# Performance work log

Hardware: AMD Instinct MI355X
Metric: run time of the kernel (lower is better)

## Reference

```python
import jax, jax.numpy as jnp
import numpy as np
import math

B, S, D = 1, 4096, 512
H, KVH, DH = 8, 4, 64
DH2 = DH // 2
M = int(math.isqrt(S))           # product-key grid side, S == M*M
K = 8                            # top_k
ROPE_BASE = 10000.0


def rope_cos_sin(seq_len, dh, base):
    inv_freq = 1.0 / (base ** (jnp.arange(0, dh, 2, dtype=jnp.float32) / dh))
    t = jnp.arange(seq_len, dtype=jnp.float32)
    freqs = jnp.outer(t, inv_freq)                      # (S, dh/2)
    emb = jnp.concatenate([freqs, freqs], axis=-1)      # (S, dh)
    return jnp.cos(emb), jnp.sin(emb)


def apply_rope(x, cos, sin):
    # x: (B, H, S, dh); half-split rotation (llama-style)
    dh2 = x.shape[-1] // 2
    rot = jnp.concatenate([-x[..., dh2:], x[..., :dh2]], axis=-1)
    return x * cos + rot * sin


def setup_inputs() -> dict:
    key = jax.random.key(0)
    ks = jax.random.split(key, 5)
    s = 0.02
    x = jax.random.normal(ks[0], (B, S, D), dtype=jnp.float32)
    Wq = jax.random.normal(ks[1], (H * DH, D), dtype=jnp.float32) * s
    Wk = jax.random.normal(ks[2], (KVH * DH, D), dtype=jnp.float32) * s
    Wv = jax.random.normal(ks[3], (KVH * DH, D), dtype=jnp.float32) * s
    Wo = jax.random.normal(ks[4], (D, H * DH), dtype=jnp.float32) * s
    return {"x": x, "Wq": Wq, "Wk": Wk, "Wv": Wv, "Wo": Wo}


def reference(x, Wq, Wk, Wv, Wo):
    b, s, d = x.shape
    cos, sin = rope_cos_sin(s, DH, ROPE_BASE)
    q = (x @ Wq.T).reshape(b, s, H, DH).transpose(0, 2, 1, 3)      # (B,H,S,DH)
    k = (x @ Wk.T).reshape(b, s, KVH, DH).transpose(0, 2, 1, 3)    # (B,KVH,S,DH)
    v = (x @ Wv.T).reshape(b, s, KVH, DH).transpose(0, 2, 1, 3)
    q = apply_rope(q, cos, sin)
    k = apply_rope(k, cos, sin)
    rep = H // KVH                                                 # GQA repeat_kv
    k = jnp.repeat(k, rep, axis=1)                                 # (B,H,S,DH)
    v = jnp.repeat(v, rep, axis=1)

    # factorized product keys: sum over grid rows / cols
    kg = k.reshape(b, H, M, M, DH)
    k1 = kg[..., :DH2].sum(axis=-2)                                # (B,H,M,DH2)
    k2 = kg[..., DH2:].sum(axis=-3)                                # (B,H,M,DH2)
    q1, q2 = q[..., :DH2], q[..., DH2:]

    def topk_sel(qh, kh):  # qh: (S,DH2), kh: (M,DH2)
        scores = qh @ kh.T                                         # (S,M)
        _, idx = jax.lax.top_k(scores, K)                          # (S,K)
        return kh[idx], idx                                        # (S,K,DH2), (S,K)

    sel2 = jax.vmap(jax.vmap(topk_sel))
    k1v, i1 = sel2(q1, k1)                                         # (B,H,S,K,DH2)
    k2v, i2 = sel2(q2, k2)

    # cross-product candidates: (B,H,S,K,K,DH) -> (B,H,S,K*K,DH)
    c1 = jnp.broadcast_to(k1v[:, :, :, :, None, :], (b, H, s, K, K, DH2))
    c2 = jnp.broadcast_to(k2v[:, :, :, None, :, :], (b, H, s, K, K, DH2))
    cand = jnp.concatenate([c1, c2], axis=-1).reshape(b, H, s, K * K, DH)

    scores_final = jnp.einsum('bhsd,bhscd->bhsc', q, cand)         # (B,H,S,K*K)
    _, sel = jax.lax.top_k(scores_final, K)                        # (B,H,S,K)
    final_k = jnp.take_along_axis(cand, sel[..., None], axis=3)    # (B,H,S,K,DH)

    row = jnp.take_along_axis(i1, sel // K, axis=3)
    col = jnp.take_along_axis(i2, sel % K, axis=3)
    v_idx = row * M + col                                          # (B,H,S,K)
    final_v = jax.vmap(jax.vmap(lambda vb, ib: vb[ib]))(v, v_idx)  # (B,H,S,K,DH)

    attn = jax.nn.softmax(
        jnp.einsum('bhsd,bhskd->bhsk', q, final_k) / math.sqrt(DH), axis=-1)
    o = jnp.einsum('bhsk,bhskd->bhsd', attn, final_v)              # (B,H,S,DH)
    o = o.transpose(0, 2, 1, 3).reshape(b, s, H * DH)
    return o @ Wo.T
```

## Files before the change

### kernel.cpp

```cpp
#include <hip/hip_runtime.h>
#include <math.h>


static constexpr size_t OFF_P1   = 0;
static constexpr size_t OFF_P2   = 4194304;
static constexpr size_t OFF_KB   = 8388608;
static constexpr size_t OFF_V    = 9437184;
static constexpr size_t OFF_COS  = 10485760;
static constexpr size_t OFF_SIN  = 10616832;
static constexpr size_t OFF_K1   = 10747904;
static constexpr size_t OFF_K2   = 10756096;
static constexpr size_t OFF_O    = 10764288;
static constexpr size_t OFF_PACK = 12861440;

#define LDB 132
#define TILE_F (16 * LDB)

__device__ __forceinline__ float rdlane_f(float v, int lane) {
  return __int_as_float(__builtin_amdgcn_readlane(__float_as_int(v), lane));
}

__global__ __launch_bounds__(512) void pre_kernel(const float* __restrict__ A,
    const float* __restrict__ Wq, const float* __restrict__ Wk,
    const float* __restrict__ Wv, float* __restrict__ C1,
    float* __restrict__ C2, float* __restrict__ cosT,
    float* __restrict__ sinT) {
  __shared__ float As[2 * TILE_F];
  __shared__ float Bs[2 * TILE_F];
  const int bid = blockIdx.x;
  const int tid = threadIdx.x;
  if (bid >= 512) {
    int idx = (bid - 512) * 512 + tid;
    int s = idx >> 5;
    int dp = idx & 31;
    double e = (double)dp * (1.0 / 32.0);
    float pf = (float)pow(10000.0, e);
    float invf = 1.0f / pf;
    float argf = __fmul_rn((float)s, invf);
    cosT[idx] = (float)cos((double)argf);
    sinT[idx] = (float)sin((double)argf);
    return;
  }
  const int bn = bid & 7;
  const int bm = (bid >> 3) & 31;
  const int z = bid >> 8;
  const int k0 = z ? 384 : 0;
  const int k1 = z ? 512 : 384;
  float* __restrict__ C = z ? C2 : C1;
  const int lrow = tid >> 2;
  const int lko = (tid & 3) << 2;
  const int ty = tid >> 4;
  const int tx = tid & 15;
  const float* Bbase = (bn < 4) ? (Wq + ((size_t)bn * 128) * 512)
                     : (bn < 6) ? (Wk + ((size_t)(bn - 4) * 128) * 512)
                                : (Wv + ((size_t)(bn - 6) * 128) * 512);
  const float* Ap = A + (size_t)(bm * 128 + lrow) * 512 + lko;
  const float* Bp = Bbase + (size_t)lrow * 512 + lko;
  float acc[4][8] = {{0.f}};
  float4 a0 = *(const float4*)(Ap + k0);
  float4 b0 = *(const float4*)(Bp + k0);
  int p = 0;
  for (int kt = k0; kt < k1; kt += 16) {
    float* Asp = As + p * TILE_F;
    float* Bsp = Bs + p * TILE_F;
    Asp[(lko + 0) * LDB + lrow] = a0.x;
    Asp[(lko + 1) * LDB + lrow] = a0.y;
    Asp[(lko + 2) * LDB + lrow] = a0.z;
    Asp[(lko + 3) * LDB + lrow] = a0.w;
    Bsp[(lko + 0) * LDB + lrow] = b0.x;
    Bsp[(lko + 1) * LDB + lrow] = b0.y;
    Bsp[(lko + 2) * LDB + lrow] = b0.z;
    Bsp[(lko + 3) * LDB + lrow] = b0.w;
    __syncthreads();
    if (kt + 16 < k1) {
      a0 = *(const float4*)(Ap + kt + 16);
      b0 = *(const float4*)(Bp + kt + 16);
    }
    #pragma unroll
    for (int k = 0; k < 16; ++k) {
      float4 av = *(const float4*)(&Asp[k * LDB + (ty << 2)]);
      float4 bl = *(const float4*)(&Bsp[k * LDB + (tx << 2)]);
      float4 bh = *(const float4*)(&Bsp[k * LDB + 64 + (tx << 2)]);
      float af[4] = {av.x, av.y, av.z, av.w};
      float bf[8] = {bl.x, bl.y, bl.z, bl.w, bh.x, bh.y, bh.z, bh.w};
      #pragma unroll
      for (int i2 = 0; i2 < 4; ++i2)
        #pragma unroll
        for (int j2 = 0; j2 < 8; ++j2)
          acc[i2][j2] = fmaf(af[i2], bf[j2], acc[i2][j2]);
    }
    p ^= 1;
  }
  #pragma unroll
  for (int i2 = 0; i2 < 4; ++i2) {
    int row = bm * 128 + (ty << 2) + i2;
    float* Cp = C + (size_t)row * 1024 + bn * 128;
    *(float4*)(Cp + (tx << 2))      = make_float4(acc[i2][0], acc[i2][1], acc[i2][2], acc[i2][3]);
    *(float4*)(Cp + 64 + (tx << 2)) = make_float4(acc[i2][4], acc[i2][5], acc[i2][6], acc[i2][7]);
  }
}

__global__ __launch_bounds__(256) void gemm128_out(const float* __restrict__ A,
    const float* __restrict__ B, float* __restrict__ Cbase, int N) {
  __shared__ float As[2 * TILE_F];
  __shared__ float Bs[2 * TILE_F];
  const int tid = threadIdx.x;
  const int z = blockIdx.z;
  const int k0 = z << 7;
  const int k1 = k0 + 128;
  float* __restrict__ C = Cbase + (size_t)z * ((size_t)4096 * N);
  const int bm = blockIdx.y, bn = blockIdx.x;
  const int lrow = tid >> 1;
  const int lko = (tid & 1) << 3;
  const int ty = tid >> 4;
  const int tx = tid & 15;
  const float* Ap = A + (size_t)(bm * 128 + lrow) * 512 + lko;
  const float* Bp = B + (size_t)(bn * 128 + lrow) * 512 + lko;
  float acc[8][8] = {{0.f}};
  float4 a0 = *(const float4*)(Ap + k0);
  float4 a1 = *(const float4*)(Ap + k0 + 4);
  float4 b0 = *(const float4*)(Bp + k0);
  float4 b1 = *(const float4*)(Bp + k0 + 4);
  int p = 0;
  for (int kt = k0; kt < k1; kt += 16) {
    float* Asp = As + p * TILE_F;
    float* Bsp = Bs + p * TILE_F;
    Asp[(lko + 0) * LDB + lrow] = a0.x;
    Asp[(lko + 1) * LDB + lrow] = a0.y;
    Asp[(lko + 2) * LDB + lrow] = a0.z;
    Asp[(lko + 3) * LDB + lrow] = a0.w;
    Asp[(lko + 4) * LDB + lrow] = a1.x;
    Asp[(lko + 5) * LDB + lrow] = a1.y;
    Asp[(lko + 6) * LDB + lrow] = a1.z;
    Asp[(lko + 7) * LDB + lrow] = a1.w;
    Bsp[(lko + 0) * LDB + lrow] = b0.x;
    Bsp[(lko + 1) * LDB + lrow] = b0.y;
    Bsp[(lko + 2) * LDB + lrow] = b0.z;
    Bsp[(lko + 3) * LDB + lrow] = b0.w;
    Bsp[(lko + 4) * LDB + lrow] = b1.x;
    Bsp[(lko + 5) * LDB + lrow] = b1.y;
    Bsp[(lko + 6) * LDB + lrow] = b1.z;
    Bsp[(lko + 7) * LDB + lrow] = b1.w;
    __syncthreads();
    if (kt + 16 < k1) {
      a0 = *(const float4*)(Ap + kt + 16);
      a1 = *(const float4*)(Ap + kt + 20);
      b0 = *(const float4*)(Bp + kt + 16);
      b1 = *(const float4*)(Bp + kt + 20);
    }
    #pragma unroll
    for (int k = 0; k < 16; ++k) {
      float4 al = *(const float4*)(&Asp[k * LDB + (ty << 2)]);
      float4 ah = *(const float4*)(&Asp[k * LDB + 64 + (ty << 2)]);
      float4 bl = *(const float4*)(&Bsp[k * LDB + (tx << 2)]);
      float4 bh = *(const float4*)(&Bsp[k * LDB + 64 + (tx << 2)]);
      float af[8] = {al.x, al.y, al.z, al.w, ah.x, ah.y, ah.z, ah.w};
      float bf[8] = {bl.x, bl.y, bl.z, bl.w, bh.x, bh.y, bh.z, bh.w};
      #pragma unroll
      for (int i2 = 0; i2 < 8; ++i2)
        #pragma unroll
        for (int j2 = 0; j2 < 8; ++j2)
          acc[i2][j2] = fmaf(af[i2], bf[j2], acc[i2][j2]);
    }
    p ^= 1;
  }
  #pragma unroll
  for (int i2 = 0; i2 < 8; ++i2) {
    int row = bm * 128 + ((i2 < 4) ? (ty << 2) + i2 : 64 + (ty << 2) + i2 - 4);
    float* Cp = C + (size_t)row * N + bn * 128;
    *(float4*)(Cp + (tx << 2))      = make_float4(acc[i2][0], acc[i2][1], acc[i2][2], acc[i2][3]);
    *(float4*)(Cp + 64 + (tx << 2)) = make_float4(acc[i2][4], acc[i2][5], acc[i2][6], acc[i2][7]);
  }
}

__global__ __launch_bounds__(256) void combine4_kernel(const float* __restrict__ o0,
    const float* __restrict__ o1, const float* __restrict__ o2,
    const float* __restrict__ o3, float* __restrict__ out) {
  int i = blockIdx.x * 256 + threadIdx.x;
  float4 a = ((const float4*)o0)[i];
  float4 b = ((const float4*)o1)[i];
  float4 c = ((const float4*)o2)[i];
  float4 d = ((const float4*)o3)[i];
  float4 r;
  r.x = __fadd_rn(__fadd_rn(__fadd_rn(a.x, b.x), c.x), d.x);
  r.y = __fadd_rn(__fadd_rn(__fadd_rn(a.y, b.y), c.y), d.y);
  r.z = __fadd_rn(__fadd_rn(__fadd_rn(a.z, b.z), c.z), d.z);
  r.w = __fadd_rn(__fadd_rn(__fadd_rn(a.w, b.w), c.w), d.w);
  ((float4*)out)[i] = r;
}

__global__ __launch_bounds__(64) void k12_rope_kernel(const float* __restrict__ p1,
    const float* __restrict__ p2, const float* __restrict__ cosT,
    const float* __restrict__ sinT, float* __restrict__ k1t,
    float* __restrict__ k2t) {
  int id = blockIdx.x * 64 + threadIdx.x;
  int which = id >> 13;
  int rem = id & 8191;
  int kvh = rem >> 11;
  int rem2 = rem & 2047;
  int i = rem2 >> 5;
  int d = rem2 & 31;
  if (which == 0) {
    float acc = 0.f;
    for (int c = 0; c < 64; ++c) {
      int s = i * 64 + c;
      int idx = (s << 10) + 512 + (kvh << 6) + d;
      float val = __fadd_rn(p1[idx], p2[idx]);
      float pv  = __fadd_rn(p1[idx + 32], p2[idx + 32]);
      float cs = cosT[(s << 5) + d];
      float sn = sinT[(s << 5) + d];
      float out = __fadd_rn(__fmul_rn(val, cs), __fmul_rn(-pv, sn));
      acc = (c == 0) ? out : __fadd_rn(acc, out);
    }
    k1t[(kvh * 64 + i) * 32 + d] = acc;
  } else {
    float acc = 0.f;
    for (int r = 0; r < 64; ++r) {
      int s = r * 64 + i;
      int idx = (s << 10) + 512 + (kvh << 6) + d + 32;
      float val = __fadd_rn(p1[idx], p2[idx]);
      float pv  = __fadd_rn(p1[idx - 32], p2[idx - 32]);
      float cs = cosT[(s << 5) + d];
      float sn = sinT[(s << 5) + d];
      float out = __fadd_rn(__fmul_rn(val, cs), __fmul_rn(pv, sn));
      acc = (r == 0) ? out : __fadd_rn(acc, out);
    }
    k2t[(kvh * 64 + i) * 32 + d] = acc;
  }
}

__global__ __launch_bounds__(256) void stage1_sel_kernel(
    const float* __restrict__ p1, const float* __restrict__ p2,
    const float* __restrict__ cosT, const float* __restrict__ sinT,
    const float* __restrict__ k1t, const float* __restrict__ k2t,
    unsigned long long* __restrict__ packs, float* __restrict__ vb) {
  __shared__ float smem[8704];
  const int bid = blockIdx.x;
  const int t = threadIdx.x;
  if (bid >= 512) {
    int vid = (bid - 512) * 256 + t;
    int s = vid >> 6;
    int g = vid & 63;
    int n = 768 + (g << 2);
    int idx = (s << 10) + n;
    const float4 v1 = *(const float4*)(p1 + idx);
    const float4 v2 = *(const float4*)(p2 + idx);
    float4 r;
    r.x = __fadd_rn(v1.x, v2.x);
    r.y = __fadd_rn(v1.y, v2.y);
    r.z = __fadd_rn(v1.z, v2.z);
    r.w = __fadd_rn(v1.w, v2.w);
    int kvh = (n - 768) >> 6;
    int d0 = n & 63;
    *(float4*)(vb + (((size_t)(kvh * 4096 + s)) << 6) + d0) = r;
    return;
  }
  float* qs = smem;
  float* kd = smem + 4352;
  const int h = bid >> 6;
  const int s0 = (bid & 63) * 64;
  const int kvh = h >> 1;
  #pragma unroll
  for (int i = 0; i < 16; ++i) {
    int j = t + i * 256;
    int ss = j >> 6, d = j & 63;
    int s = s0 + ss;
    int idx = (s << 10) + (h << 6) + d;
    float val = __fadd_rn(p1[idx], p2[idx]);
    float pv  = __fadd_rn(p1[idx ^ 32], p2[idx ^ 32]);
    float cs = cosT[(s << 5) + (d & 31)];
    float sn = sinT[(s << 5) + (d & 31)];
    float rot = (d < 32) ? -pv : pv;
    qs[d * 68 + ss] = __fadd_rn(__fmul_rn(val, cs), __fmul_rn(rot, sn));
  }
  #pragma unroll
  for (int i = 0; i < 8; ++i) {
    int j = t + i * 256;
    int r = j >> 5, d = j & 31;
    kd[d * 132 + r]      = k1t[(kvh * 64 + r) * 32 + d];
    kd[d * 132 + 64 + r] = k2t[(kvh * 64 + r) * 32 + d];
  }
  __syncthreads();
  const int ty = t >> 4;
  const int tx = t & 15;
  float acc1[4][4] = {{0.f}};
  float acc2[4][4] = {{0.f}};
  #pragma unroll
  for (int dp = 0; dp < 32; ++dp) {
    float4 kv1 = *(const float4*)&kd[dp * 132 + (ty << 2)];
    float4 kv2 = *(const float4*)&kd[dp * 132 + 64 + (ty << 2)];
    float4 q1 = *(const float4*)&qs[dp * 68 + (tx << 2)];
    float4 q2 = *(const float4*)&qs[(32 + dp) * 68 + (tx << 2)];
    float k1f[4] = {kv1.x, kv1.y, kv1.z, kv1.w};
    float k2f[4] = {kv2.x, kv2.y, kv2.z, kv2.w};
    float q1f[4] = {q1.x, q1.y, q1.z, q1.w};
    float q2f[4] = {q2.x, q2.y, q2.z, q2.w};
    #pragma unroll
    for (int i2 = 0; i2 < 4; ++i2)
      #pragma unroll
      for (int j2 = 0; j2 < 4; ++j2) {
        acc1[i2][j2] = fmaf(k1f[i2], q1f[j2], acc1[i2][j2]);
        acc2[i2][j2] = fmaf(k2f[i2], q2f[j2], acc2[i2][j2]);
      }
  }
  __syncthreads();
  float* sct = smem;
  #pragma unroll
  for (int i2 = 0; i2 < 4; ++i2) {
    int r = (ty << 2) + i2;
    *(float4*)&sct[(size_t)r * 68 + (tx << 2)] =
        make_float4(acc1[i2][0], acc1[i2][1], acc1[i2][2], acc1[i2][3]);
    *(float4*)&sct[(size_t)(64 + r) * 68 + (tx << 2)] =
        make_float4(acc2[i2][0], acc2[i2][1], acc2[i2][2], acc2[i2][3]);
  }
  __syncthreads();
  if (t < 128) {
    int set = t >> 6;
    int sq = t & 63;
    const float* p = sct + (size_t)(set << 6) * 68 + sq;
    float top[8];
    int idx[8];
    #pragma unroll
    for (int u = 0; u < 8; ++u) { top[u] = -INFINITY; idx[u] = 0; }
    #pragma unroll
    for (int r = 0; r < 64; ++r) {
      float v = p[(size_t)r * 68];
      int i = r;
      #pragma unroll
      for (int j = 0; j < 8; ++j) {
        bool gt = v > top[j];
        float tv = top[j]; int ti = idx[j];
        top[j] = gt ? v : tv;
        idx[j] = gt ? i : ti;
        v = gt ? tv : v;
        i = gt ? ti : i;
      }
    }
    unsigned long long pp = 0;
    #pragma unroll
    for (int u = 0; u < 8; ++u) pp |= (unsigned long long)idx[u] << (6 * u);
    packs[(((size_t)(h * 4096 + s0 + sq)) << 1) + set] = pp;
  }
}

__device__ __forceinline__ void bitonic64_val_desc(float& v, int lane) {
  #pragma unroll
  for (int k = 2; k <= 64; k <<= 1) {
    #pragma unroll
    for (int j = k >> 1; j >= 1; j >>= 1) {
      float ov = __shfl_xor(v, j, 64);
      bool up = ((lane & k) == 0) == ((lane & j) == 0);
      float mx = fmaxf(v, ov), mn = fminf(v, ov);
      v = up ? mx : mn;
    }
  }
}

__global__ __launch_bounds__(256) void attn_sel2_kernel(
    const ulonglong2* __restrict__ packs, const float* __restrict__ p1,
    const float* __restrict__ p2, const float* __restrict__ cosT,
    const float* __restrict__ sinT, const float* __restrict__ vb,
    const float* __restrict__ k1t, const float* __restrict__ k2t,
    float* __restrict__ ob) {
  const int lane = threadIdx.x & 63;
  const int w = blockIdx.x * 4 + (threadIdx.x >> 6);
  const int h = w >> 12;
  const int s = w & 4095;
  const int kvh = h >> 1;
  ulonglong2 pk = packs[w];
  const unsigned long long pack1 = pk.x, pack2 = pk.y;
  int qidx = (s << 10) + (h << 6) + lane;
  float vraw = __fadd_rn(p1[qidx], p2[qidx]);
  float pv = __shfl_xor(vraw, 32, 64);
  float cs = cosT[(s << 5) + (lane & 31)];
  float sn = sinT[(s << 5) + (lane & 31)];
  float rot = (lane < 32) ? -pv : pv;
  const float qv = __fadd_rn(__fmul_rn(vraw, cs), __fmul_rn(rot, sn));

  int r1 = (int)((pack1 >> (6 * (lane >> 3))) & 63);
  int r2 = (int)((pack2 >> (6 * (lane & 7))) & 63);
  const float* k1p = k1t + (size_t)(kvh * 64 + r1) * 32;
  const float* k2p = k2t + (size_t)(kvh * 64 + r2) * 32;
  float c = 0.f;
  #pragma unroll
  for (int dq = 0; dq < 32; dq += 4) {
    float4 kk = *(const float4*)(k1p + dq);
    c = __fadd_rn(c, __fmul_rn(rdlane_f(qv, dq + 0), kk.x));
    c = __fadd_rn(c, __fmul_rn(rdlane_f(qv, dq + 1), kk.y));
    c = __fadd_rn(c, __fmul_rn(rdlane_f(qv, dq + 2), kk.z));
    c = __fadd_rn(c, __fmul_rn(rdlane_f(qv, dq + 3), kk.w));
  }
  #pragma unroll
  for (int dq = 0; dq < 32; dq += 4) {
    float4 kk = *(const float4*)(k2p + dq);
    c = __fadd_rn(c, __fmul_rn(rdlane_f(qv, 32 + dq + 0), kk.x));
    c = __fadd_rn(c, __fmul_rn(rdlane_f(qv, 32 + dq + 1), kk.y));
    c = __fadd_rn(c, __fmul_rn(rdlane_f(qv, 32 + dq + 2), kk.z));
    c = __fadd_rn(c, __fmul_rn(rdlane_f(qv, 32 + dq + 3), kk.w));
  }
  const float scand = c;
  float v3 = c;
  bitonic64_val_desc(v3, lane);
  float cvs[8]; int ccs[8];
  unsigned long long used = 0;
  #pragma unroll
  for (int t = 0; t < 8; ++t) {
    float tv = rdlane_f(v3, t);
    unsigned long long m = __ballot(scand == tv) & ~used;
    int ix = __ffsll((long long)m) - 1;
    used |= 1ull << ix;
    cvs[t] = tv;
    ccs[t] = ix;
  }
  float y[8];
  #pragma unroll
  for (int t = 0; t < 8; ++t) y[t] = cvs[t] * 0.125f;
  float mx = y[0];
  #pragma unroll
  for (int t = 1; t < 8; ++t) if (y[t] > mx) mx = y[t];
  float e[8];
  #pragma unroll
  for (int t = 0; t < 8; ++t) e[t] = __expf(__fsub_rn(y[t], mx));
  float wsum = __fadd_rn(__fadd_rn(__fadd_rn(e[0], e[1]), __fadd_rn(e[2], e[3])),
                         __fadd_rn(__fadd_rn(e[4], e[5]), __fadd_rn(e[6], e[7])));
  const float* vbh = vb + ((size_t)kvh << 18);
  float o = 0.f;
  #pragma unroll
  for (int t = 0; t < 8; ++t) {
    float att = __fdiv_rn(e[t], wsum);
    int row = (int)((pack1 >> (6 * (ccs[t] >> 3))) & 63);
    int col = (int)((pack2 >> (6 * (ccs[t] & 7))) & 63);
    o = __fadd_rn(o, __fmul_rn(att, vbh[((size_t)(row * 64 + col) << 6) + lane]));
  }
  ob[(size_t)s * 512 + (h << 6) + lane] = o;
}

extern "C" void kernel_launch(void* const* d_in, const int* in_sizes, int n_in,
                              void* d_out, int out_size, void* d_ws, size_t ws_size,
                              hipStream_t stream) {
  const float* x  = (const float*)d_in[0];
  const float* Wq = (const float*)d_in[1];
  const float* Wk = (const float*)d_in[2];
  const float* Wv = (const float*)d_in[3];
  const float* Wo = (const float*)d_in[4];
  float* ws = (float*)d_ws;
  float* p1   = ws + OFF_P1;
  float* p2   = ws + OFF_P2;
  float* vb   = ws + OFF_V;
  float* cosT = ws + OFF_COS;
  float* sinT = ws + OFF_SIN;
  float* k1t  = ws + OFF_K1;
  float* k2t  = ws + OFF_K2;
  float* ob   = ws + OFF_O;
  unsigned long long* packs = (unsigned long long*)(ws + OFF_PACK);
  float* op = ws + OFF_P1;

  pre_kernel<<<768, 512, 0, stream>>>(x, Wq, Wk, Wv, p1, p2, cosT, sinT);
  k12_rope_kernel<<<256, 64, 0, stream>>>(p1, p2, cosT, sinT, k1t, k2t);
  stage1_sel_kernel<<<1536, 256, 0, stream>>>(p1, p2, cosT, sinT, k1t, k2t,
                                              packs, vb);
  attn_sel2_kernel<<<8192, 256, 0, stream>>>((const ulonglong2*)packs, p1, p2,
                                             cosT, sinT, vb, k1t, k2t, ob);
  gemm128_out<<<dim3(4, 32, 4), 256, 0, stream>>>(ob, Wo, op, 512);
  combine4_kernel<<<2048, 256, 0, stream>>>(op, op + 2097152, op + 4194304,
                                            op + 6291456, (float*)d_out);
}
```

Before: 226.0 us.

## Compute V projection with split-bf16 MFMA in pre_kernel, drop V repack pass

```diff
diff --git a/kernel.cpp b/kernel.cpp
--- a/kernel.cpp
+++ b/kernel.cpp
@@ -1,10 +1,10 @@
 #include <hip/hip_runtime.h>
+#include <hip/hip_bf16.h>
 #include <math.h>
 
 
 static constexpr size_t OFF_P1   = 0;
 static constexpr size_t OFF_P2   = 4194304;
-static constexpr size_t OFF_KB   = 8388608;
 static constexpr size_t OFF_V    = 9437184;
 static constexpr size_t OFF_COS  = 10485760;
 static constexpr size_t OFF_SIN  = 10616832;
@@ -16,17 +16,27 @@
 #define LDB 132
 #define TILE_F (16 * LDB)
 
+typedef __attribute__((ext_vector_type(8))) short short8v;
+typedef __attribute__((ext_vector_type(4))) float float4v;
+
 __device__ __forceinline__ float rdlane_f(float v, int lane) {
   return __int_as_float(__builtin_amdgcn_readlane(__float_as_int(v), lane));
+}
+
+__device__ __forceinline__ void bf16_split(float x, short& hi, short& lo) {
+  __hip_bfloat16 h = __float2bfloat16(x);
+  float back = __bfloat162float(h);
+  __hip_bfloat16 l = __float2bfloat16(__fsub_rn(x, back));
+  hi = *reinterpret_cast<short*>(&h);
+  lo = *reinterpret_cast<short*>(&l);
 }
 
 __global__ __launch_bounds__(512) void pre_kernel(const float* __restrict__ A,
     const float* __restrict__ Wq, const float* __restrict__ Wk,
     const float* __restrict__ Wv, float* __restrict__ C1,
     float* __restrict__ C2, float* __restrict__ cosT,
-    float* __restrict__ sinT) {
-  __shared__ float As[2 * TILE_F];
-  __shared__ float Bs[2 * TILE_F];
+    float* __restrict__ sinT, float* __restrict__ vb) {
+  __shared__ float smem[9216];
   const int bid = blockIdx.x;
   const int tid = threadIdx.x;
   if (bid >= 512) {
@@ -41,9 +51,88 @@
     sinT[idx] = (float)sin((double)argf);
     return;
   }
-  const int bn = bid & 7;
-  const int bm = (bid >> 3) & 31;
-  const int z = bid >> 8;
+  if (bid >= 384) {
+    const int bv = bid - 384;
+    const int bmv = bv & 31;
+    const int bnv = bv >> 5;
+    const int wid = tid >> 6;
+    const int lane = tid & 63;
+    const int m0 = bmv * 128;
+    const int n0 = bnv * 64;
+    const int lr = lane & 15;
+    const int lk = (lane >> 4) << 3;
+    float* xs = smem;
+    const int sr = tid >> 2;
+    const int sc = (tid & 3) << 3;
+    const float* Sp = A + (size_t)(m0 + sr) * 512 + sc;
+    const float* Wvp = Wv + (size_t)(n0 + lr) * 512 + lk;
+    float4v acc0 = {0.f, 0.f, 0.f, 0.f};
+    float4v acc1 = {0.f, 0.f, 0.f, 0.f};
+    float4v acc2 = {0.f, 0.f, 0.f, 0.f};
+    float4v acc3 = {0.f, 0.f, 0.f, 0.f};
+    float4 g0 = *(const float4*)(Sp);
+    float4 g1 = *(const float4*)(Sp + 4);
+    int p = 0;
+    for (int kt = 0; kt < 512; kt += 32) {
+      float* xsp = xs + p * 4608;
+      *(float4*)&xsp[sr * 36 + sc]     = g0;
+      *(float4*)&xsp[sr * 36 + sc + 4] = g1;
+      __syncthreads();
+      if (kt + 32 < 512) {
+        g0 = *(const float4*)(Sp + kt + 32);
+        g1 = *(const float4*)(Sp + kt + 36);
+      }
+      const float* ap = &xsp[(wid * 16 + lr) * 36 + lk];
+      float4 a0 = *(const float4*)ap;
+      float4 a1 = *(const float4*)(ap + 4);
+      float av[8] = {a0.x, a0.y, a0.z, a0.w, a1.x, a1.y, a1.z, a1.w};
+      short8v ah, al;
+      #pragma unroll
+      for (int e = 0; e < 8; ++e) {
+        short h, l;
+        bf16_split(av[e], h, l);
+        ah[e] = h;
+        al[e] = l;
+      }
+      #pragma unroll
+      for (int j = 0; j < 4; ++j) {
+        float4 w0 = *(const float4*)(Wvp + (size_t)j * 16 * 512 + kt);
+        float4 w1 = *(const float4*)(Wvp + (size_t)j * 16 * 512 + kt + 4);
+        float wv[8] = {w0.x, w0.y, w0.z, w0.w, w1.x, w1.y, w1.z, w1.w};
+        short8v bh, bl;
+        #pragma unroll
+        for (int e = 0; e < 8; ++e) {
+          short h, l;
+          bf16_split(wv[e], h, l);
+          bh[e] = h;
+          bl[e] = l;
+        }
+        float4v* accp = (j == 0) ? &acc0 : (j == 1) ? &acc1 : (j == 2) ? &acc2 : &acc3;
+        *accp = __builtin_amdgcn_mfma_f32_16x16x32_bf16(ah, bh, *accp, 0, 0, 0);
+        *accp = __builtin_amdgcn_mfma_f32_16x16x32_bf16(al, bh, *accp, 0, 0, 0);
+        *accp = __builtin_amdgcn_mfma_f32_16x16x32_bf16(ah, bl, *accp, 0, 0, 0);
+      }
+      p ^= 1;
+    }
+    const int rbase = m0 + wid * 16 + ((lane >> 4) << 2);
+    #pragma unroll
+    for (int j = 0; j < 4; ++j) {
+      float4v accv = (j == 0) ? acc0 : (j == 1) ? acc1 : (j == 2) ? acc2 : acc3;
+      int n = n0 + j * 16 + (lane & 15);
+      int kvh = n >> 6;
+      int d = n & 63;
+      #pragma unroll
+      for (int r = 0; r < 4; ++r)
+        vb[((size_t)(kvh * 4096 + rbase + r)) * 64 + d] = accv[r];
+    }
+    return;
+  }
+  float* As = smem;
+  float* Bs = smem + 2 * TILE_F;
+  const int z = bid / 192;
+  const int pid = bid - z * 192;
+  const int bn = pid % 6;
+  const int bm = pid / 6;
   const int k0 = z ? 384 : 0;
   const int k1 = z ? 512 : 384;
   float* __restrict__ C = z ? C2 : C1;
@@ -52,8 +141,7 @@
   const int ty = tid >> 4;
   const int tx = tid & 15;
   const float* Bbase = (bn < 4) ? (Wq + ((size_t)bn * 128) * 512)
-                     : (bn < 6) ? (Wk + ((size_t)(bn - 4) * 128) * 512)
-                                : (Wv + ((size_t)(bn - 6) * 128) * 512);
+                                : (Wk + ((size_t)(bn - 4) * 128) * 512);
   const float* Ap = A + (size_t)(bm * 128 + lrow) * 512 + lko;
   const float* Bp = Bbase + (size_t)lrow * 512 + lko;
   float acc[4][8] = {{0.f}};
@@ -202,6 +290,7 @@
   int d = rem2 & 31;
   if (which == 0) {
     float acc = 0.f;
+    #pragma unroll 8
     for (int c = 0; c < 64; ++c) {
       int s = i * 64 + c;
       int idx = (s << 10) + 512 + (kvh << 6) + d;
@@ -215,6 +304,7 @@
     k1t[(kvh * 64 + i) * 32 + d] = acc;
   } else {
     float acc = 0.f;
+    #pragma unroll 8
     for (int r = 0; r < 64; ++r) {
       int s = r * 64 + i;
       int idx = (s << 10) + 512 + (kvh << 6) + d + 32;
@@ -233,28 +323,10 @@
     const float* __restrict__ p1, const float* __restrict__ p2,
     const float* __restrict__ cosT, const float* __restrict__ sinT,
     const float* __restrict__ k1t, const float* __restrict__ k2t,
-    unsigned long long* __restrict__ packs, float* __restrict__ vb) {
+    unsigned long long* __restrict__ packs) {
   __shared__ float smem[8704];
   const int bid = blockIdx.x;
   const int t = threadIdx.x;
-  if (bid >= 512) {
-    int vid = (bid - 512) * 256 + t;
-    int s = vid >> 6;
-    int g = vid & 63;
-    int n = 768 + (g << 2);
-    int idx = (s << 10) + n;
-    const float4 v1 = *(const float4*)(p1 + idx);
-    const float4 v2 = *(const float4*)(p2 + idx);
-    float4 r;
-    r.x = __fadd_rn(v1.x, v2.x);
-    r.y = __fadd_rn(v1.y, v2.y);
-    r.z = __fadd_rn(v1.z, v2.z);
-    r.w = __fadd_rn(v1.w, v2.w);
-    int kvh = (n - 768) >> 6;
-    int d0 = n & 63;
-    *(float4*)(vb + (((size_t)(kvh * 4096 + s)) << 6) + d0) = r;
-    return;
-  }
   float* qs = smem;
   float* kd = smem + 4352;
   const int h = bid >> 6;
@@ -455,10 +527,9 @@
   unsigned long long* packs = (unsigned long long*)(ws + OFF_PACK);
   float* op = ws + OFF_P1;
 
-  pre_kernel<<<768, 512, 0, stream>>>(x, Wq, Wk, Wv, p1, p2, cosT, sinT);
+  pre_kernel<<<768, 512, 0, stream>>>(x, Wq, Wk, Wv, p1, p2, cosT, sinT, vb);
   k12_rope_kernel<<<256, 64, 0, stream>>>(p1, p2, cosT, sinT, k1t, k2t);
-  stage1_sel_kernel<<<1536, 256, 0, stream>>>(p1, p2, cosT, sinT, k1t, k2t,
-                                              packs, vb);
+  stage1_sel_kernel<<<512, 256, 0, stream>>>(p1, p2, cosT, sinT, k1t, k2t, packs);
   attn_sel2_kernel<<<8192, 256, 0, stream>>>((const ulonglong2*)packs, p1, p2,
                                              cosT, sinT, vb, k1t, k2t, ob);
   gemm128_out<<<dim3(4, 32, 4), 256, 0, stream>>>(ob, Wo, op, 512);
```

Measured after the change: 248.4 us. 9.9% more time.
